# Optimization experiments

Measured on AMD Instinct MI355X. Metric: run time of the kernel, lower is better.

## Reference

```python
import jax, jax.numpy as jnp
import numpy as np

D = 512
H = 8
DH = D // H
EPS = 1e-5


def _layernorm(x, g, b):
    mu = jnp.mean(x, axis=-1, keepdims=True)
    var = jnp.mean((x - mu) ** 2, axis=-1, keepdims=True)
    return (x - mu) * jax.lax.rsqrt(var + EPS) * g + b


def setup_inputs() -> dict:
    key = jax.random.key(0)
    ks = jax.random.split(key, 10)
    B, S = 4, 2048
    s = 1.0 / np.sqrt(D)
    return {
        "x": jax.random.normal(ks[0], (B, S, D), dtype=jnp.float32),
        "Wq": jax.random.normal(ks[1], (D, D), dtype=jnp.float32) * s,
        "Wk": jax.random.normal(ks[2], (D, D), dtype=jnp.float32) * s,
        "Wv": jax.random.normal(ks[3], (D, D), dtype=jnp.float32) * s,
        "Wo": jax.random.normal(ks[4], (D, D), dtype=jnp.float32) * s,
        "W1": jax.random.normal(ks[5], (4 * D, D), dtype=jnp.float32) * s,
        "b1": jnp.zeros((4 * D,), dtype=jnp.float32),
        "W2": jax.random.normal(ks[6], (D, 4 * D), dtype=jnp.float32) * (1.0 / np.sqrt(4 * D)),
        "b2": jnp.zeros((D,), dtype=jnp.float32),
        "g1": jnp.ones((D,), dtype=jnp.float32),
        "bb1": jnp.zeros((D,), dtype=jnp.float32),
        "g2": jnp.ones((D,), dtype=jnp.float32),
        "bb2": jnp.zeros((D,), dtype=jnp.float32),
    }


def reference(x, Wq, Wk, Wv, Wo, W1, b1, W2, b2, g1, bb1, g2, bb2):
    B, S, _ = x.shape
    # projections (torch Linear: y = x @ W.T), split heads: chunk(-1) == reshape to [B,S,H,DH]
    q = (x @ Wq.T).reshape(B, S, H, DH).transpose(0, 2, 1, 3)  # [B,H,S,DH]
    k = (x @ Wk.T).reshape(B, S, H, DH).transpose(0, 2, 1, 3)
    v = (x @ Wv.T).reshape(B, S, H, DH).transpose(0, 2, 1, 3)
    scores = jnp.einsum("bhsd,bhtd->bhst", q, k) / np.sqrt(DH)  # [B,H,S,S]
    attn = jax.nn.softmax(scores, axis=-1)
    ctx = jnp.einsum("bhst,bhtd->bhsd", attn, v)  # [B,H,S,DH]
    ctx = ctx.transpose(0, 2, 1, 3).reshape(B, S, D)
    h = _layernorm(x + ctx @ Wo.T, g1, bb1)
    mlp = jax.nn.relu(h @ W1.T + b1) @ W2.T + b2
    return _layernorm(h + mlp, g2, bb2)
```

## Files before the change

### kernel.cpp

```cpp
#include <hip/hip_runtime.h>
#include <hip/hip_bf16.h>
#include <cstdint>
#include <cstddef>

typedef short bf16x8 __attribute__((ext_vector_type(8)));
typedef float floatx4 __attribute__((ext_vector_type(4)));
typedef unsigned short u16;

constexpr int B = 4, S = 2048, D = 512, H = 8, DH = 64;
constexpr int M_ROWS = B * S;
constexpr int D4 = 4 * D;
constexpr float QSCALE = 0.18033688011112042f;

__device__ __forceinline__ u16 f2b(float f) {
  unsigned u = __builtin_bit_cast(unsigned, f);
  u += 0x7fff + ((u >> 16) & 1);
  return (u16)(u >> 16);
}

__device__ __forceinline__ bf16x8 ldfrag(const u16* p) {
  return *reinterpret_cast<const bf16x8*>(p);
}

__device__ __forceinline__ floatx4 mfma16(bf16x8 a, bf16x8 b, floatx4 c) {
  return __builtin_amdgcn_mfma_f32_16x16x32_bf16(a, b, c, 0, 0, 0);
}

__device__ __forceinline__ ushort4 f2b4(float4 v) {
  ushort4 r;
  r.x = f2b(v.x); r.y = f2b(v.y); r.z = f2b(v.z); r.w = f2b(v.w);
  return r;
}

__device__ __forceinline__ void gld16(const u16* g, u16* l) {
  __builtin_amdgcn_global_load_lds(
      (const __attribute__((address_space(1))) void*)g,
      (__attribute__((address_space(3))) void*)l, 16, 0, 0);
}

__global__ void cast_all_kernel(const float4* __restrict__ x,
                                const float4* __restrict__ w1, const float4* __restrict__ w2,
                                const float4* __restrict__ wq, const float4* __restrict__ wk,
                                const float4* __restrict__ wv, const float4* __restrict__ wo,
                                ushort4* __restrict__ xb,
                                ushort4* __restrict__ w1b, ushort4* __restrict__ w2b,
                                ushort4* __restrict__ wqb, ushort4* __restrict__ wkb,
                                ushort4* __restrict__ wvb, ushort4* __restrict__ wob) {
  int i = blockIdx.x * blockDim.x + threadIdx.x;
  constexpr int NX = (M_ROWS * D) / 4;
  constexpr int N1 = (D4 * D) / 4;
  constexpr int NS = (D * D) / 4;
  if (i < NX) { xb[i] = f2b4(x[i]); return; }
  i -= NX;
  if (i < N1) { w1b[i] = f2b4(w1[i]); return; }
  i -= N1;
  if (i < N1) { w2b[i] = f2b4(w2[i]); return; }
  i -= N1;
  const int sel = i >> 16, off = i & (NS - 1);
  const float4* src = sel == 0 ? wq : sel == 1 ? wk : sel == 2 ? wv : wo;
  ushort4* dst = sel == 0 ? wqb : sel == 1 ? wkb : sel == 2 ? wvb : wob;
  dst[off] = f2b4(src[off]);
}

template <int EPI>
__global__ __launch_bounds__(256) void gemm_bt(
    const u16* __restrict__ A, const u16* __restrict__ W,
    const float* __restrict__ bias, void* __restrict__ out0, void* __restrict__ out1,
    int M, int N, int K, int klen) {
  __shared__ __align__(16) u16 As[2][128 * 32];
  __shared__ __align__(16) u16 Bs[2][128 * 32];
  const int wave = threadIdx.x >> 6, lane = threadIdx.x & 63;
  const int quad = lane >> 4, l16 = lane & 15;
  const int rowB = blockIdx.y * 128, colB = blockIdx.x * 128;
  const int rowW = (wave >> 1) * 64, colW = (wave & 1) * 64;
  const int koff = blockIdx.z * klen;
  void* out = blockIdx.z ? out1 : out0;

  floatx4 acc[4][4];
#pragma unroll
  for (int i = 0; i < 4; i++)
#pragma unroll
    for (int j = 0; j < 4; j++) acc[i][j] = (floatx4){0.f,0.f,0.f,0.f};

  const u16* gA = A + (size_t)(rowB + wave * 32 + (lane >> 2)) * K + koff + (lane & 3) * 8;
  const u16* gB = W + (size_t)(colB + wave * 32 + (lane >> 2)) * K + koff + (lane & 3) * 8;
  const int lds_off = wave * 1024;

#pragma unroll
  for (int rr = 0; rr < 2; rr++) {
    gld16(gA + (size_t)rr * 16 * K, &As[0][lds_off + rr * 512]);
    gld16(gB + (size_t)rr * 16 * K, &Bs[0][lds_off + rr * 512]);
  }

  int buf = 0;
  for (int kc = 0; kc < klen; kc += 32, buf ^= 1) {
    __syncthreads();

    if (kc + 32 < klen) {
#pragma unroll
      for (int rr = 0; rr < 2; rr++) {
        gld16(gA + (size_t)rr * 16 * K + kc + 32, &As[buf ^ 1][lds_off + rr * 512]);
        gld16(gB + (size_t)rr * 16 * K + kc + 32, &Bs[buf ^ 1][lds_off + rr * 512]);
      }
    }

    bf16x8 a[4], b[4];
#pragma unroll
    for (int i = 0; i < 4; i++)
      a[i] = ldfrag(&As[buf][(rowW + i * 16 + l16) * 32 + quad * 8]);
#pragma unroll
    for (int j = 0; j < 4; j++)
      b[j] = ldfrag(&Bs[buf][(colW + j * 16 + l16) * 32 + quad * 8]);
#pragma unroll
    for (int i = 0; i < 4; i++)
#pragma unroll
      for (int j = 0; j < 4; j++) acc[i][j] = mfma16(a[i], b[j], acc[i][j]);
  }

#pragma unroll
  for (int i = 0; i < 4; i++) {
#pragma unroll
    for (int j = 0; j < 4; j++) {
      const int gn = colB + colW + j * 16 + l16;
      const float bv = (EPI == 1) ? bias[gn] : 0.f;
#pragma unroll
      for (int r = 0; r < 4; r++) {
        const int gm = rowB + rowW + i * 16 + quad * 4 + r;
        float v = acc[i][j][r] + bv;
        if (EPI == 0) {
          ((float*)out)[(size_t)gm * N + gn] = v;
        } else {
          v = v > 0.f ? v : 0.f;
          ((u16*)out)[(size_t)gm * N + gn] = f2b(v);
        }
      }
    }
  }
}

__global__ __launch_bounds__(256) void qkv_gemm(
    const u16* __restrict__ xb,
    const u16* __restrict__ wq, const u16* __restrict__ wk, const u16* __restrict__ wv,
    u16* __restrict__ q, u16* __restrict__ k, u16* __restrict__ vT) {
  __shared__ __align__(16) u16 As[2][128 * 32];
  __shared__ __align__(16) u16 Bs[2][128 * 32];
  const int which = blockIdx.z;
  const u16* __restrict__ W = which == 0 ? wq : (which == 1 ? wk : wv);
  const int wave = threadIdx.x >> 6, lane = threadIdx.x & 63;
  const int quad = lane >> 4, l16 = lane & 15;
  const int rowB = blockIdx.y * 128, colB = blockIdx.x * 128;
  const int rowW = (wave >> 1) * 64, colW = (wave & 1) * 64;

  floatx4 acc[4][4];
#pragma unroll
  for (int i = 0; i < 4; i++)
#pragma unroll
    for (int j = 0; j < 4; j++) acc[i][j] = (floatx4){0.f,0.f,0.f,0.f};

  const u16* gA = xb + (size_t)(rowB + wave * 32 + (lane >> 2)) * D + (lane & 3) * 8;
  const u16* gB = W + (size_t)(colB + wave * 32 + (lane >> 2)) * D + (lane & 3) * 8;
  const int lds_off = wave * 1024;

#pragma unroll
  for (int rr = 0; rr < 2; rr++) {
    gld16(gA + (size_t)rr * 16 * D, &As[0][lds_off + rr * 512]);
    gld16(gB + (size_t)rr * 16 * D, &Bs[0][lds_off + rr * 512]);
  }

  int buf = 0;
  for (int kc = 0; kc < D; kc += 32, buf ^= 1) {
    __syncthreads();

    if (kc + 32 < D) {
#pragma unroll
      for (int rr = 0; rr < 2; rr++) {
        gld16(gA + (size_t)rr * 16 * D + kc + 32, &As[buf ^ 1][lds_off + rr * 512]);
        gld16(gB + (size_t)rr * 16 * D + kc + 32, &Bs[buf ^ 1][lds_off + rr * 512]);
      }
    }

    bf16x8 a[4], b[4];
#pragma unroll
    for (int i = 0; i < 4; i++)
      a[i] = ldfrag(&As[buf][(rowW + i * 16 + l16) * 32 + quad * 8]);
#pragma unroll
    for (int j = 0; j < 4; j++)
      b[j] = ldfrag(&Bs[buf][(colW + j * 16 + l16) * 32 + quad * 8]);
#pragma unroll
    for (int i = 0; i < 4; i++)
#pragma unroll
      for (int j = 0; j < 4; j++) acc[i][j] = mfma16(a[i], b[j], acc[i][j]);
  }

  const float oscale = (which == 0) ? QSCALE : 1.0f;
  u16* dst01 = which == 0 ? q : k;
#pragma unroll
  for (int i = 0; i < 4; i++) {
#pragma unroll
    for (int j = 0; j < 4; j++) {
      const int gn = colB + colW + j * 16 + l16;
      const int h = gn >> 6, dh = gn & 63;
#pragma unroll
      for (int r = 0; r < 4; r++) {
        const int gm = rowB + rowW + i * 16 + quad * 4 + r;
        const int bb = gm >> 11, s = gm & 2047;
        const u16 val = f2b(acc[i][j][r] * oscale);
        if (which < 2) {
          dst01[((((size_t)bb * H + h) * S) + s) * DH + dh] = val;
        } else {
          vT[((((size_t)bb * H + h) * DH) + dh) * S + s] = val;
        }
      }
    }
  }
}

constexpr int PST = 72;

__global__ __launch_bounds__(512, 1) void attn_kernel(
    const u16* __restrict__ q, const u16* __restrict__ k,
    const u16* __restrict__ vT, u16* __restrict__ ctxb) {
  __shared__ __align__(16) u16 kvlds[2][2][2][2][64 * 32];
  __shared__ __align__(16) u16 plds[8][64 * PST];
  const int wave = threadIdx.x >> 6, lane = threadIdx.x & 63;
  const int quad = lane >> 4, l16 = lane & 15;
  const int pair = wave >> 1, khalf = wave & 1;
  const int blk = (blockIdx.x & 7) * 32 + (blockIdx.x >> 3);
  const int w = blk * 4 + pair;
  const int bh = w >> 5, qt = w & 31;
  const int bb = bh >> 3, h = bh & 7;

  const u16* qp = q + ((size_t)bh * S + qt * 64 + l16) * DH + quad * 8;
  bf16x8 qf[4][2];
#pragma unroll
  for (int t = 0; t < 4; t++) {
    qf[t][0] = ldfrag(qp + (size_t)t * 16 * DH);
    qf[t][1] = ldfrag(qp + (size_t)t * 16 * DH + 32);
  }

  const int st = pair * 64 + lane;
  const int srow = st >> 2, sp = (st & 3) * 8;
  const u16* kS = k + (size_t)bh * S * DH + (size_t)(khalf * 1024 + srow) * DH + sp;
  const u16* vS = vT + (size_t)bh * DH * S + (size_t)srow * S + khalf * 1024 + sp;

  floatx4 o[4][4];
#pragma unroll
  for (int t = 0; t < 4; t++)
#pragma unroll
    for (int c = 0; c < 4; c++) o[t][c] = (floatx4){0.f,0.f,0.f,0.f};
  float lacc[4] = {0.f, 0.f, 0.f, 0.f};

  u16* myp = plds[wave];
  u16* wpb = myp + l16 * PST + quad * 4;
  const u16* rpb = myp + l16 * PST + quad * 8;

  gld16(kS, &kvlds[0][khalf][0][0][pair * 512]);
  gld16(kS + 32, &kvlds[0][khalf][0][1][pair * 512]);
  gld16(vS, &kvlds[0][khalf][1][0][pair * 512]);
  gld16(vS + 32, &kvlds[0][khalf][1][1][pair * 512]);

  int buf = 0;
  for (int kt = 0; kt < S / 2; kt += 64, buf ^= 1) {
    __syncthreads();

    bf16x8 kf[8], vf[8];
#pragma unroll
    for (int i = 0; i < 4; i++) {
      kf[2 * i]     = ldfrag(&kvlds[buf][khalf][0][0][(i * 16 + l16) * 32 + quad * 8]);
      kf[2 * i + 1] = ldfrag(&kvlds[buf][khalf][0][1][(i * 16 + l16) * 32 + quad * 8]);
      vf[2 * i]     = ldfrag(&kvlds[buf][khalf][1][0][(i * 16 + l16) * 32 + quad * 8]);
      vf[2 * i + 1] = ldfrag(&kvlds[buf][khalf][1][1][(i * 16 + l16) * 32 + quad * 8]);
    }

    if (kt + 64 < S / 2) {
      const int nb = buf ^ 1;
      gld16(kS + (size_t)(kt + 64) * DH, &kvlds[nb][khalf][0][0][pair * 512]);
      gld16(kS + (size_t)(kt + 64) * DH + 32, &kvlds[nb][khalf][0][1][pair * 512]);
      gld16(vS + kt + 64, &kvlds[nb][khalf][1][0][pair * 512]);
      gld16(vS + kt + 96, &kvlds[nb][khalf][1][1][pair * 512]);
    }

#pragma unroll
    for (int t = 0; t < 4; t++) {
      floatx4 sc[4];
#pragma unroll
      for (int i = 0; i < 4; i++) {
        floatx4 z = (floatx4){0.f,0.f,0.f,0.f};
        z = mfma16(kf[2 * i], qf[t][0], z);
        z = mfma16(kf[2 * i + 1], qf[t][1], z);
        sc[i] = z;
      }
      float a = 0.f;
#pragma unroll
      for (int i = 0; i < 4; i++) {
        const float p0 = __builtin_amdgcn_exp2f(sc[i][0]);
        const float p1 = __builtin_amdgcn_exp2f(sc[i][1]);
        const float p2 = __builtin_amdgcn_exp2f(sc[i][2]);
        const float p3 = __builtin_amdgcn_exp2f(sc[i][3]);
        a += (p0 + p1) + (p2 + p3);
        const unsigned lo = __builtin_amdgcn_perm(
            __builtin_bit_cast(unsigned, p1) + 0x8000u,
            __builtin_bit_cast(unsigned, p0) + 0x8000u, 0x07060302u);
        const unsigned hi = __builtin_amdgcn_perm(
            __builtin_bit_cast(unsigned, p3) + 0x8000u,
            __builtin_bit_cast(unsigned, p2) + 0x8000u, 0x07060302u);
        uint2 pk; pk.x = lo; pk.y = hi;
        *reinterpret_cast<uint2*>(&wpb[t * 16 * PST + i * 16]) = pk;
      }
      lacc[t] += a;
    }

#pragma unroll
    for (int t = 0; t < 4; t++) {
      const bf16x8 pf0 = ldfrag(rpb + (size_t)t * 16 * PST);
      const bf16x8 pf1 = ldfrag(rpb + (size_t)t * 16 * PST + 32);
#pragma unroll
      for (int c = 0; c < 4; c++) {
        o[t][c] = mfma16(pf0, vf[2 * c], o[t][c]);
        o[t][c] = mfma16(pf1, vf[2 * c + 1], o[t][c]);
      }
    }
  }

  float lt[4];
#pragma unroll
  for (int t = 0; t < 4; t++) {
    float l = lacc[t];
    l += __shfl_xor(l, 16);
    l += __shfl_xor(l, 32);
    lt[t] = l;
  }

  float* ob = reinterpret_cast<float*>(plds[2 * pair]);
  float* lb0 = ob + 64 * 64;
  float* lb1 = lb0 + 64;

  __syncthreads();
  if (quad == 0) {
    float* dst = khalf ? lb1 : lb0;
#pragma unroll
    for (int t = 0; t < 4; t++) dst[t * 16 + l16] = lt[t];
  }
  if (khalf == 1) {
#pragma unroll
    for (int t = 0; t < 4; t++)
#pragma unroll
      for (int c = 0; c < 4; c++)
        *reinterpret_cast<floatx4*>(&ob[lane * 64 + (t * 4 + c) * 4]) = o[t][c];
  }
  __syncthreads();
  if (khalf == 0) {
    float inv[4][4];
#pragma unroll
    for (int t = 0; t < 4; t++)
#pragma unroll
      for (int r = 0; r < 4; r++)
        inv[t][r] = 1.0f / (lb0[t * 16 + quad * 4 + r] + lb1[t * 16 + quad * 4 + r]);

    const size_t crow_base = ((size_t)bb * S) * D + h * DH;
#pragma unroll
    for (int t = 0; t < 4; t++)
#pragma unroll
      for (int c = 0; c < 4; c++) {
        const floatx4 oo = o[t][c] +
            *reinterpret_cast<const floatx4*>(&ob[lane * 64 + (t * 4 + c) * 4]);
        const int dh = c * 16 + l16;
#pragma unroll
        for (int r = 0; r < 4; r++) {
          const int s = qt * 64 + t * 16 + quad * 4 + r;
          ctxb[crow_base + (size_t)s * D + dh] = f2b(oo[r] * inv[t][r]);
        }
      }
  }
}

template <int MODE>
__global__ __launch_bounds__(256) void ln_kernel(
    const void* __restrict__ resid, const float* __restrict__ ya,
    const float* __restrict__ yb, const float* __restrict__ pb,
    const float* __restrict__ g, const float* __restrict__ bvec,
    float* __restrict__ outF, u16* __restrict__ outB) {
  const int wave = threadIdx.x >> 6, lane = threadIdx.x & 63;
  const int row = blockIdx.x * 4 + wave;
  const float* ap = ya + (size_t)row * D + lane * 8;
  const float* bp = yb + (size_t)row * D + lane * 8;
  float v[8];
  const float4 a0 = *(const float4*)ap, a1 = *(const float4*)(ap + 4);
  const float4 b0 = *(const float4*)bp, b1 = *(const float4*)(bp + 4);
  v[0] = a0.x + b0.x; v[1] = a0.y + b0.y; v[2] = a0.z + b0.z; v[3] = a0.w + b0.w;
  v[4] = a1.x + b1.x; v[5] = a1.y + b1.y; v[6] = a1.z + b1.z; v[7] = a1.w + b1.w;
  if (MODE == 0) {
    const float* rp = (const float*)resid + (size_t)row * D + lane * 8;
    const float4 r0 = *(const float4*)rp, r1 = *(const float4*)(rp + 4);
    v[0] += r0.x; v[1] += r0.y; v[2] += r0.z; v[3] += r0.w;
    v[4] += r1.x; v[5] += r1.y; v[6] += r1.z; v[7] += r1.w;
  } else {
    const u16* rp = (const u16*)resid + (size_t)row * D + lane * 8;
    const ushort4 h0 = *(const ushort4*)rp, h1 = *(const ushort4*)(rp + 4);
    v[0] += __builtin_bit_cast(float, (unsigned)h0.x << 16);
    v[1] += __builtin_bit_cast(float, (unsigned)h0.y << 16);
    v[2] += __builtin_bit_cast(float, (unsigned)h0.z << 16);
    v[3] += __builtin_bit_cast(float, (unsigned)h0.w << 16);
    v[4] += __builtin_bit_cast(float, (unsigned)h1.x << 16);
    v[5] += __builtin_bit_cast(float, (unsigned)h1.y << 16);
    v[6] += __builtin_bit_cast(float, (unsigned)h1.z << 16);
    v[7] += __builtin_bit_cast(float, (unsigned)h1.w << 16);
    const float4 p0 = *(const float4*)(pb + lane * 8);
    const float4 p1 = *(const float4*)(pb + lane * 8 + 4);
    v[0] += p0.x; v[1] += p0.y; v[2] += p0.z; v[3] += p0.w;
    v[4] += p1.x; v[5] += p1.y; v[6] += p1.z; v[7] += p1.w;
  }
  float sum = 0.f;
#pragma unroll
  for (int i = 0; i < 8; i++) sum += v[i];
#pragma unroll
  for (int d = 1; d < 64; d <<= 1) sum += __shfl_xor(sum, d);
  const float mu = sum * (1.f / D);
  float vs = 0.f;
#pragma unroll
  for (int i = 0; i < 8; i++) { const float t = v[i] - mu; vs += t * t; }
#pragma unroll
  for (int d = 1; d < 64; d <<= 1) vs += __shfl_xor(vs, d);
  const float rstd = rsqrtf(vs * (1.f / D) + 1e-5f);
#pragma unroll
  for (int i = 0; i < 8; i++) {
    const int col = lane * 8 + i;
    const float o = (v[i] - mu) * rstd * g[col] + bvec[col];
    if (MODE == 0) outB[(size_t)row * D + col] = f2b(o);
    else           outF[(size_t)row * D + col] = o;
  }
}

constexpr size_t OFF_XB  = 0;
constexpr size_t OFF_WQB = 8u << 20;
constexpr size_t OFF_WKB = OFF_WQB + (512u << 10);
constexpr size_t OFF_WVB = OFF_WKB + (512u << 10);
constexpr size_t OFF_WOB = OFF_WVB + (512u << 10);
constexpr size_t OFF_W1B = 10u << 20;
constexpr size_t OFF_W2B = 12u << 20;
constexpr size_t OFF_Q   = 14u << 20;
constexpr size_t OFF_K   = 22u << 20;
constexpr size_t OFF_VT  = 30u << 20;
constexpr size_t OFF_CTX = 38u << 20;
constexpr size_t OFF_Y   = 46u << 20;
constexpr size_t OFF_HB  = 78u << 20;
constexpr size_t OFF_M1B = 86u << 20;

extern "C" void kernel_launch(void* const* d_in, const int* in_sizes, int n_in,
                              void* d_out, int out_size, void* d_ws, size_t ws_size,
                              hipStream_t stream) {
  const float* x  = (const float*)d_in[0];
  const float* Wq = (const float*)d_in[1];
  const float* Wk = (const float*)d_in[2];
  const float* Wv = (const float*)d_in[3];
  const float* Wo = (const float*)d_in[4];
  const float* W1 = (const float*)d_in[5];
  const float* b1 = (const float*)d_in[6];
  const float* W2 = (const float*)d_in[7];
  const float* b2 = (const float*)d_in[8];
  const float* g1 = (const float*)d_in[9];
  const float* bb1 = (const float*)d_in[10];
  const float* g2 = (const float*)d_in[11];
  const float* bb2 = (const float*)d_in[12];

  char* ws = (char*)d_ws;
  u16* xb  = (u16*)(ws + OFF_XB);
  u16* wqb = (u16*)(ws + OFF_WQB);
  u16* wkb = (u16*)(ws + OFF_WKB);
  u16* wvb = (u16*)(ws + OFF_WVB);
  u16* wob = (u16*)(ws + OFF_WOB);
  u16* w1b = (u16*)(ws + OFF_W1B);
  u16* w2b = (u16*)(ws + OFF_W2B);
  u16* qb  = (u16*)(ws + OFF_Q);
  u16* kb  = (u16*)(ws + OFF_K);
  u16* vtb = (u16*)(ws + OFF_VT);
  u16* ctxb = (u16*)(ws + OFF_CTX);
  float* y0 = (float*)(ws + OFF_Y);
  float* y1 = (float*)(ws + OFF_Q);
  u16* hb  = (u16*)(ws + OFF_HB);
  u16* m1b = (u16*)(ws + OFF_M1B);

  {
    const int n4 = (M_ROWS * D) / 4 + (D4 * D) / 4 * 2 + (D * D) / 4 * 4;
    cast_all_kernel<<<(n4 + 255) / 256, 256, 0, stream>>>(
        (const float4*)x, (const float4*)W1, (const float4*)W2, (const float4*)Wq,
        (const float4*)Wk, (const float4*)Wv, (const float4*)Wo,
        (ushort4*)xb, (ushort4*)w1b, (ushort4*)w2b, (ushort4*)wqb,
        (ushort4*)wkb, (ushort4*)wvb, (ushort4*)wob);
  }

  qkv_gemm<<<dim3(D / 128, M_ROWS / 128, 3), 256, 0, stream>>>(xb, wqb, wkb, wvb, qb, kb, vtb);

  attn_kernel<<<B * H * S / 64 / 4, 512, 0, stream>>>(qb, kb, vtb, ctxb);

  gemm_bt<0><<<dim3(D / 128, M_ROWS / 128, 2), 256, 0, stream>>>(
      ctxb, wob, nullptr, y0, y1, M_ROWS, D, D, D / 2);

  ln_kernel<0><<<M_ROWS / 4, 256, 0, stream>>>(
      x, y0, y1, nullptr, g1, bb1, nullptr, hb);

  gemm_bt<1><<<dim3(D4 / 128, M_ROWS / 128, 1), 256, 0, stream>>>(
      hb, w1b, b1, m1b, nullptr, M_ROWS, D4, D, D);

  gemm_bt<0><<<dim3(D / 128, M_ROWS / 128, 2), 256, 0, stream>>>(
      m1b, w2b, nullptr, y0, y1, M_ROWS, D, D4, D4 / 2);

  ln_kernel<1><<<M_ROWS / 4, 256, 0, stream>>>(
      hb, y0, y1, b2, g2, bb2, (float*)d_out, nullptr);
}
```

Before: 261.7 us.

## Keep softmax probabilities in registers by permuting V layout, drop P LDS staging

The QKV projection now writes V^T with a permuted sequence index within each 64-block. The exp'd score fragments from the QK^T MFMA can then be packed straight into the A operand of the PV MFMA without a round trip through a per-wave LDS buffer. This removes the P write/read in shared memory and frees the plds allocation. The epilogue reuses kvlds for the cross-wave reduction with an XOR-swizzled slot to avoid bank conflicts. It also adds s_setprio around the MFMA blocks.

Measured after the change: 257.3 us. Within noise of the previous version (-1.7%).

```diff
diff --git a/kernel.cpp b/kernel.cpp
--- a/kernel.cpp
+++ b/kernel.cpp
@@ -5,6 +5,7 @@
 
 typedef short bf16x8 __attribute__((ext_vector_type(8)));
 typedef float floatx4 __attribute__((ext_vector_type(4)));
+typedef unsigned int uintx4 __attribute__((ext_vector_type(4)));
 typedef unsigned short u16;
 
 constexpr int B = 4, S = 2048, D = 512, H = 8, DH = 64;
@@ -208,20 +209,20 @@
         if (which < 2) {
           dst01[((((size_t)bb * H + h) * S) + s) * DH + dh] = val;
         } else {
-          vT[((((size_t)bb * H + h) * DH) + dh) * S + s] = val;
+          const int sl = s & 63;
+          const int sw = (s & ~63) | (sl & 35) | ((sl & 12) << 1) | ((sl & 16) >> 2);
+          vT[((((size_t)bb * H + h) * DH) + dh) * S + sw] = val;
         }
       }
     }
   }
 }
-
-constexpr int PST = 72;
 
 __global__ __launch_bounds__(512, 1) void attn_kernel(
     const u16* __restrict__ q, const u16* __restrict__ k,
     const u16* __restrict__ vT, u16* __restrict__ ctxb) {
   __shared__ __align__(16) u16 kvlds[2][2][2][2][64 * 32];
-  __shared__ __align__(16) u16 plds[8][64 * PST];
+  __shared__ __align__(16) float ltb[2][4][64];
   const int wave = threadIdx.x >> 6, lane = threadIdx.x & 63;
   const int quad = lane >> 4, l16 = lane & 15;
   const int pair = wave >> 1, khalf = wave & 1;
@@ -250,10 +251,6 @@
     for (int c = 0; c < 4; c++) o[t][c] = (floatx4){0.f,0.f,0.f,0.f};
   float lacc[4] = {0.f, 0.f, 0.f, 0.f};
 
-  u16* myp = plds[wave];
-  u16* wpb = myp + l16 * PST + quad * 4;
-  const u16* rpb = myp + l16 * PST + quad * 8;
-
   gld16(kS, &kvlds[0][khalf][0][0][pair * 512]);
   gld16(kS + 32, &kvlds[0][khalf][0][1][pair * 512]);
   gld16(vS, &kvlds[0][khalf][1][0][pair * 512]);
@@ -283,6 +280,7 @@
 #pragma unroll
     for (int t = 0; t < 4; t++) {
       floatx4 sc[4];
+      __builtin_amdgcn_s_setprio(1);
 #pragma unroll
       for (int i = 0; i < 4; i++) {
         floatx4 z = (floatx4){0.f,0.f,0.f,0.f};
@@ -290,6 +288,9 @@
         z = mfma16(kf[2 * i + 1], qf[t][1], z);
         sc[i] = z;
       }
+      __builtin_amdgcn_s_setprio(0);
+
+      unsigned wd[8];
       float a = 0.f;
 #pragma unroll
       for (int i = 0; i < 4; i++) {
@@ -298,27 +299,26 @@
         const float p2 = __builtin_amdgcn_exp2f(sc[i][2]);
         const float p3 = __builtin_amdgcn_exp2f(sc[i][3]);
         a += (p0 + p1) + (p2 + p3);
-        const unsigned lo = __builtin_amdgcn_perm(
+        wd[2 * i] = __builtin_amdgcn_perm(
             __builtin_bit_cast(unsigned, p1) + 0x8000u,
             __builtin_bit_cast(unsigned, p0) + 0x8000u, 0x07060302u);
-        const unsigned hi = __builtin_amdgcn_perm(
+        wd[2 * i + 1] = __builtin_amdgcn_perm(
             __builtin_bit_cast(unsigned, p3) + 0x8000u,
             __builtin_bit_cast(unsigned, p2) + 0x8000u, 0x07060302u);
-        uint2 pk; pk.x = lo; pk.y = hi;
-        *reinterpret_cast<uint2*>(&wpb[t * 16 * PST + i * 16]) = pk;
       }
       lacc[t] += a;
-    }
-
-#pragma unroll
-    for (int t = 0; t < 4; t++) {
-      const bf16x8 pf0 = ldfrag(rpb + (size_t)t * 16 * PST);
-      const bf16x8 pf1 = ldfrag(rpb + (size_t)t * 16 * PST + 32);
+      const uintx4 lo4 = (uintx4){wd[0], wd[1], wd[2], wd[3]};
+      const uintx4 hi4 = (uintx4){wd[4], wd[5], wd[6], wd[7]};
+      const bf16x8 pa0 = __builtin_bit_cast(bf16x8, lo4);
+      const bf16x8 pa1 = __builtin_bit_cast(bf16x8, hi4);
+
+      __builtin_amdgcn_s_setprio(1);
 #pragma unroll
       for (int c = 0; c < 4; c++) {
-        o[t][c] = mfma16(pf0, vf[2 * c], o[t][c]);
-        o[t][c] = mfma16(pf1, vf[2 * c + 1], o[t][c]);
-      }
+        o[t][c] = mfma16(pa0, vf[2 * c], o[t][c]);
+        o[t][c] = mfma16(pa1, vf[2 * c + 1], o[t][c]);
+      }
+      __builtin_amdgcn_s_setprio(0);
     }
   }
 
@@ -331,22 +331,21 @@
     lt[t] = l;
   }
 
-  float* ob = reinterpret_cast<float*>(plds[2 * pair]);
-  float* lb0 = ob + 64 * 64;
-  float* lb1 = lb0 + 64;
-
   __syncthreads();
+  float* ob = reinterpret_cast<float*>(&kvlds[0][0][0][0][0]) + pair * 4096;
   if (quad == 0) {
-    float* dst = khalf ? lb1 : lb0;
-#pragma unroll
-    for (int t = 0; t < 4; t++) dst[t * 16 + l16] = lt[t];
+#pragma unroll
+    for (int t = 0; t < 4; t++) ltb[khalf][pair][t * 16 + l16] = lt[t];
   }
   if (khalf == 1) {
 #pragma unroll
     for (int t = 0; t < 4; t++)
 #pragma unroll
-      for (int c = 0; c < 4; c++)
-        *reinterpret_cast<floatx4*>(&ob[lane * 64 + (t * 4 + c) * 4]) = o[t][c];
+      for (int c = 0; c < 4; c++) {
+        const int idx = 4 * t + c;
+        const int slot = (idx & 8) | ((idx ^ (lane & 7)) & 7);
+        *reinterpret_cast<floatx4*>(&ob[lane * 64 + slot * 4]) = o[t][c];
+      }
   }
   __syncthreads();
   if (khalf == 0) {
@@ -355,15 +354,18 @@
     for (int t = 0; t < 4; t++)
 #pragma unroll
       for (int r = 0; r < 4; r++)
-        inv[t][r] = 1.0f / (lb0[t * 16 + quad * 4 + r] + lb1[t * 16 + quad * 4 + r]);
+        inv[t][r] = 1.0f / (ltb[0][pair][t * 16 + quad * 4 + r] +
+                            ltb[1][pair][t * 16 + quad * 4 + r]);
 
     const size_t crow_base = ((size_t)bb * S) * D + h * DH;
 #pragma unroll
     for (int t = 0; t < 4; t++)
 #pragma unroll
       for (int c = 0; c < 4; c++) {
+        const int idx = 4 * t + c;
+        const int slot = (idx & 8) | ((idx ^ (lane & 7)) & 7);
         const floatx4 oo = o[t][c] +
-            *reinterpret_cast<const floatx4*>(&ob[lane * 64 + (t * 4 + c) * 4]);
+            *reinterpret_cast<const floatx4*>(&ob[lane * 64 + slot * 4]);
         const int dh = c * 16 + l16;
 #pragma unroll
         for (int r = 0; r < 4; r++) {
```
